# Optimization experiments

Measured on AMD Instinct MI355X. Metric: run time of the kernel, lower is better.

The kernel has to match this reference:

```python
import jax, jax.numpy as jnp
import numpy as np

B, S, D, H, DFF = 2, 2048, 1024, 16, 4096
DK = D // H
EPS = 1e-6


def setup_inputs() -> dict:
    key = jax.random.key(0)
    ks = jax.random.split(key, 16)
    s = lambda fan_in: 1.0 / np.sqrt(fan_in)
    inp = {
        "xb": jax.random.normal(ks[0], (B, S, D), jnp.float32),
        "mask": jnp.ones((B, 1, 1, S), jnp.int32),
        "Wq": jax.random.normal(ks[1], (D, D), jnp.float32) * s(D),
        "bq": jnp.zeros((D,), jnp.float32),
        "Wk": jax.random.normal(ks[2], (D, D), jnp.float32) * s(D),
        "bk": jnp.zeros((D,), jnp.float32),
        "Wv": jax.random.normal(ks[3], (D, D), jnp.float32) * s(D),
        "bv": jnp.zeros((D,), jnp.float32),
        "Wo": jax.random.normal(ks[4], (D, D), jnp.float32) * s(D),
        "bo": jnp.zeros((D,), jnp.float32),
        "W1": jax.random.normal(ks[5], (D, DFF), jnp.float32) * s(D),
        "b1": jnp.zeros((DFF,), jnp.float32),
        "W2": jax.random.normal(ks[6], (DFF, D), jnp.float32) * s(DFF),
        "b2": jnp.zeros((D,), jnp.float32),
        "a1": jnp.ones((1,), jnp.float32),
        "o1": jnp.zeros((1,), jnp.float32),
        "a2": jnp.ones((1,), jnp.float32),
        "o2": jnp.zeros((1,), jnp.float32),
    }
    return inp


def layernorm(x, alpha, bias):
    # matches LayerNormalization: unbiased std (torch default), scalar alpha/bias,
    # division by (std + eps)
    mean = jnp.mean(x, axis=-1, keepdims=True)
    var = jnp.sum((x - mean) ** 2, axis=-1, keepdims=True) / (x.shape[-1] - 1)
    std = jnp.sqrt(var)
    return alpha * (x - mean) / (std + EPS) + bias


def mha(x, mask, Wq, bq, Wk, bk, Wv, bv, Wo, bo):
    b, s, d = x.shape
    q = (x @ Wq + bq).reshape(b, s, H, DK).transpose(0, 2, 1, 3)  # [B,H,S,DK]
    k = (x @ Wk + bk).reshape(b, s, H, DK).transpose(0, 2, 1, 3)
    v = (x @ Wv + bv).reshape(b, s, H, DK).transpose(0, 2, 1, 3)
    logits = jnp.einsum("bhqd,bhkd->bhqk", q, k) / np.sqrt(DK)
    logits = jnp.where(mask == 0, jnp.float32(-1e9), logits)
    probs = jax.nn.softmax(logits, axis=-1)
    a = jnp.einsum("bhqk,bhkd->bhqd", probs, v)  # [B,H,S,DK]
    a = a.transpose(0, 2, 1, 3).reshape(b, s, d)
    return a @ Wo + bo


def reference(xb, mask, Wq, bq, Wk, bk, Wv, bv, Wo, bo, W1, b1, W2, b2, a1, o1, a2, o2):
    # residual 1: x + MHA(LN(x))  (dropout disabled: eval mode)
    h = xb + mha(layernorm(xb, a1, o1), mask, Wq, bq, Wk, bk, Wv, bv, Wo, bo)
    # residual 2: h + FFN(LN(h))
    z = layernorm(h, a2, o2)
    ff = jax.nn.relu(z @ W1 + b1) @ W2 + b2
    return h + ff
```

## Files before the change

### kernel.cpp

```cpp
#include <hip/hip_runtime.h>
#include <hip/hip_bf16.h>
#include <math.h>

typedef __bf16 bf16x8 __attribute__((ext_vector_type(8)));
typedef float f32x4 __attribute__((ext_vector_type(4)));
typedef float f32x16 __attribute__((ext_vector_type(16)));
typedef unsigned short u16;

#define DEV __device__ __forceinline__

static constexpr int Bc = 2, Sc = 2048, Dc = 1024, Hc = 16, DFFc = 4096, DKc = 64;
static constexpr int Mc = Bc * Sc;
static constexpr float QSCALE = 0.125f * 1.4426950408889634f;

DEV u16 f32_to_bf16(float x) {
    unsigned u = __builtin_bit_cast(unsigned, x);
    u += 0x7FFFu + ((u >> 16) & 1u);
    return (u16)(u >> 16);
}

DEV float bf16_to_f32(u16 h) {
    return __builtin_bit_cast(float, (unsigned)h << 16);
}

DEV float exp2_fast(float x) {
    float r;
    asm("v_exp_f32 %0, %1" : "=v"(r) : "v"(x));
    return r;
}

DEV unsigned cvt_pk_bf16(float lo, float hi_) {
    unsigned r;
    asm("v_cvt_pk_bf16_f32 %0, %1, %2" : "=v"(r) : "v"(lo), "v"(hi_));
    return r;
}

DEV void gload_lds16(const u16* g, u16* l) {
    __builtin_amdgcn_global_load_lds(
        (const __attribute__((address_space(1))) void*)g,
        (__attribute__((address_space(3))) void*)l, 16, 0, 0);
}

DEV float block_reduce_sum(float v) {
    __shared__ float part[4];
    int lane = threadIdx.x & 63, w = threadIdx.x >> 6;
    #pragma unroll
    for (int m = 1; m < 64; m <<= 1) v += __shfl_xor(v, m);
    __syncthreads();
    if (lane == 0) part[w] = v;
    __syncthreads();
    return part[0] + part[1] + part[2] + part[3];
}

__global__ __launch_bounds__(256)
void ln_kernel(const float* __restrict__ x, u16* __restrict__ y,
               const float* __restrict__ alpha, const float* __restrict__ beta) {
    long row = blockIdx.x;
    const float4 v = reinterpret_cast<const float4*>(x + row * Dc)[threadIdx.x];
    float s = v.x + v.y + v.z + v.w;
    s = block_reduce_sum(s);
    float mean = s * (1.0f / Dc);
    float d0 = v.x - mean, d1 = v.y - mean, d2 = v.z - mean, d3 = v.w - mean;
    float ss = d0*d0 + d1*d1 + d2*d2 + d3*d3;
    ss = block_reduce_sum(ss);
    float stdv = sqrtf(ss / (float)(Dc - 1));
    float sc = alpha[0] / (stdv + 1e-6f);
    float bi = beta[0];
    ushort4 o;
    o.x = f32_to_bf16(d0 * sc + bi);
    o.y = f32_to_bf16(d1 * sc + bi);
    o.z = f32_to_bf16(d2 * sc + bi);
    o.w = f32_to_bf16(d3 * sc + bi);
    reinterpret_cast<ushort4*>(y + row * Dc)[threadIdx.x] = o;
}

__global__ void transpose_conv_kernel(const float* __restrict__ in, u16* __restrict__ out,
                                      int K, int N) {
    __shared__ float tile[32][33];
    int k0 = blockIdx.y * 32, n0 = blockIdx.x * 32;
    int tx = threadIdx.x, ty = threadIdx.y;
    #pragma unroll
    for (int i = 0; i < 4; i++)
        tile[ty + i*8][tx] = in[(long)(k0 + ty + i*8) * N + n0 + tx];
    __syncthreads();
    #pragma unroll
    for (int i = 0; i < 4; i++)
        out[(long)(n0 + ty + i*8) * K + k0 + tx] = f32_to_bf16(tile[tx][ty + i*8]);
}

__global__ __launch_bounds__(256)
void mbias_kernel(const int* __restrict__ mask, float* __restrict__ mbias) {
    int i = blockIdx.x * 256 + threadIdx.x;
    mbias[i] = mask[i] ? 0.f : -1e9f;
}

enum { EPI_QKV = 0, EPI_RELU = 1, EPI_RES = 2 };

template<int EPI, int BM, int BN, bool DB>
__global__ __launch_bounds__(256, 3)
void gemm_kernel(const u16* __restrict__ A, const u16* __restrict__ BT,
                 const float* __restrict__ b0, const float* __restrict__ b1,
                 const float* __restrict__ b2, void* __restrict__ outp,
                 const float* __restrict__ res, int M, int N, int K) {
    constexpr int BK = 64, RI = BM / 32, RJ = BN / 32;
    constexpr int NB = DB ? 2 : 1;
    __shared__ u16 As[NB][BM * BK];
    __shared__ u16 Bs[NB][BN * BK];
    const int tid = threadIdx.x;
    const int wave = tid >> 6, lane = tid & 63;
    const int wr = wave >> 1, wc = wave & 1;
    const int lr = lane & 15, lg = lane >> 4;
    const int m0 = blockIdx.y * BM, n0 = blockIdx.x * BN;
    const int z = blockIdx.z;
    const u16* Bz = BT + (size_t)z * N * K;
    const int srow = lane >> 3, scol = (lane & 7) * 8;

    f32x4 acc[RI][RJ] = {};

    const u16* ap[RI];
    const u16* bp[RJ];
    #pragma unroll
    for (int i = 0; i < RI; i++) ap[i] = A  + (size_t)(m0 + (wave*RI + i)*8 + srow) * K + scol;
    #pragma unroll
    for (int j = 0; j < RJ; j++) bp[j] = Bz + (size_t)(n0 + (wave*RJ + j)*8 + srow) * K + scol;

    auto stage = [&](int bi, int kt) {
        #pragma unroll
        for (int i = 0; i < RI; i++) gload_lds16(ap[i] + kt, &As[bi][(wave*RI + i) * 512]);
        #pragma unroll
        for (int j = 0; j < RJ; j++) gload_lds16(bp[j] + kt, &Bs[bi][(wave*RJ + j) * 512]);
    };
    auto compute = [&](int bi) {
        #pragma unroll
        for (int ks = 0; ks < BK; ks += 32) {
            bf16x8 a[RI], b[RJ];
            #pragma unroll
            for (int i = 0; i < RI; i++)
                a[i] = *reinterpret_cast<const bf16x8*>(&As[bi][(wr*(BM/2) + i*16 + lr) * BK + ks + lg*8]);
            #pragma unroll
            for (int j = 0; j < RJ; j++)
                b[j] = *reinterpret_cast<const bf16x8*>(&Bs[bi][(wc*(BN/2) + j*16 + lr) * BK + ks + lg*8]);
            #pragma unroll
            for (int i = 0; i < RI; i++)
                #pragma unroll
                for (int j = 0; j < RJ; j++)
                    acc[i][j] = __builtin_amdgcn_mfma_f32_16x16x32_bf16(a[i], b[j], acc[i][j], 0, 0, 0);
        }
    };

    if constexpr (DB) {
        const int nT = K / BK;
        stage(0, 0);
        __syncthreads();
        for (int t = 0; t < nT; t++) {
            const int cur = t & 1;
            if (t + 1 < nT) stage(cur ^ 1, (t + 1) * BK);
            compute(cur);
            __syncthreads();
        }
    } else {
        for (int kt = 0; kt < K; kt += BK) {
            stage(0, kt);
            __syncthreads();
            compute(0);
            __syncthreads();
        }
    }

    const float* bias = (EPI == EPI_QKV) ? (z == 0 ? b0 : z == 1 ? b1 : b2) : b0;
    #pragma unroll
    for (int i = 0; i < RI; i++) {
        #pragma unroll
        for (int j = 0; j < RJ; j++) {
            const int col = n0 + wc*(BN/2) + j*16 + lr;
            const float bv = bias[col];
            #pragma unroll
            for (int rg = 0; rg < 4; rg++) {
                const int row = m0 + wr*(BM/2) + i*16 + lg*4 + rg;
                float val = acc[i][j][rg] + bv;
                if constexpr (EPI == EPI_QKV) {
                    int bb = row >> 11, s = row & (Sc - 1);
                    int hh = col >> 6, dk = col & 63;
                    u16* o = (u16*)outp + (size_t)z * Mc * Dc;
                    if (z == 2)
                        o[((size_t)(bb * Hc + hh) * DKc + dk) * Sc + s] = f32_to_bf16(val);
                    else
                        o[(((size_t)(bb * Hc + hh) * Sc + s) << 6) + dk] =
                            f32_to_bf16(z == 0 ? val * QSCALE : val);
                } else if constexpr (EPI == EPI_RELU) {
                    ((u16*)outp)[(size_t)row * N + col] = f32_to_bf16(fmaxf(val, 0.0f));
                } else {
                    size_t idx = (size_t)row * N + col;
                    ((float*)outp)[idx] = res[idx] + val;
                }
            }
        }
    }
}

__global__ __launch_bounds__(256, 4)
void attn_kernel(const u16* __restrict__ Qg, const u16* __restrict__ Kg,
                 const u16* __restrict__ VTg, const float* __restrict__ mbias,
                 u16* __restrict__ part, float2* __restrict__ ml) {
    constexpr int KVB = 64, NT = (Sc / 2) / KVB;
    __shared__ u16 Ks[2][KVB * DKc];
    __shared__ u16 VTs[2][KVB * DKc];
    __shared__ float mbs[Sc / 2];

    const int tid = threadIdx.x;
    const int wave = tid >> 6, lane = tid & 63;
    const int l31 = lane & 31, hi = lane >> 5;
    const int bh = blockIdx.y, b = bh >> 4, hh = bh & 15;
    const int q0 = blockIdx.x * 128 + wave * 32;
    const int z = blockIdx.z, kv0 = z * (Sc / 2);
    const long base = (long)bh * Sc * DKc;

    *reinterpret_cast<float4*>(&mbs[tid * 4]) =
        *reinterpret_cast<const float4*>(&mbias[b * Sc + kv0 + tid * 4]);

    bf16x8 qf[4];
    {
        const u16* qrow = Qg + base + (long)(q0 + l31) * DKc + hi * 8;
        #pragma unroll
        for (int s = 0; s < 4; s++)
            qf[s] = *reinterpret_cast<const bf16x8*>(qrow + s * 16);
    }

    const int unit0 = wave * 128 + lane;
    const int r0 = unit0 >> 3, u0 = unit0 & 7;
    const int c8 = (u0 ^ (r0 & 7)) * 8;
    const u16* ksrc = Kg  + base + (size_t)(kv0 + r0) * DKc + c8;
    const u16* vsrc = VTg + base + (size_t)r0 * Sc + kv0 + c8;

    auto stage = [&](int bi, int kt) {
        gload_lds16(ksrc + (size_t)kt * DKc,       &Ks [bi][wave * 1024]);
        gload_lds16(ksrc + (size_t)(kt + 8) * DKc, &Ks [bi][wave * 1024 + 512]);
        gload_lds16(vsrc + kt,                     &VTs[bi][wave * 1024]);
        gload_lds16(vsrc + kt + 8 * Sc,            &VTs[bi][wave * 1024 + 512]);
    };

    stage(0, 0);
    __syncthreads();

    f32x16 accO[2] = {};
    float mrun = -3.0e38f, lrun = 0.f;

    for (int t = 0; t < NT; t++) {
        const int cur = t & 1;
        if (t + 1 < NT) stage(cur ^ 1, (t + 1) * KVB);

        f32x16 st[2];
        #pragma unroll
        for (int kt2 = 0; kt2 < 2; kt2++) {
            f32x16 s = {};
            const int row = kt2 * 32 + l31;
            #pragma unroll
            for (int step = 0; step < 4; step++) {
                const int unit = (step * 2 + hi) ^ (row & 7);
                bf16x8 kf = *reinterpret_cast<const bf16x8*>(&Ks[cur][row * DKc + unit * 8]);
                s = __builtin_amdgcn_mfma_f32_32x32x16_bf16(kf, qf[step], s, 0, 0, 0);
            }
            st[kt2] = s;
        }

        float pm = -3.0e38f;
        #pragma unroll
        for (int kt2 = 0; kt2 < 2; kt2++) {
            #pragma unroll
            for (int g = 0; g < 4; g++) {
                const float4 mb = *reinterpret_cast<const float4*>(
                    &mbs[t * KVB + kt2 * 32 + g * 8 + hi * 4]);
                st[kt2][g*4+0] += mb.x;
                st[kt2][g*4+1] += mb.y;
                st[kt2][g*4+2] += mb.z;
                st[kt2][g*4+3] += mb.w;
                pm = fmaxf(fmaxf(pm, st[kt2][g*4+0]), st[kt2][g*4+1]);
                pm = fmaxf(fmaxf(pm, st[kt2][g*4+2]), st[kt2][g*4+3]);
            }
        }
        pm = fmaxf(pm, __shfl_xor(pm, 32));

        if (__any(pm - mrun > 11.54f)) {
            const float mnew = fmaxf(mrun, pm);
            const float corr = exp2_fast(mrun - mnew);
            mrun = mnew; lrun *= corr;
            #pragma unroll
            for (int r = 0; r < 16; r++) {
                accO[0][r] *= corr;
                accO[1][r] *= corr;
            }
        }

        float rsum = 0.f;
        #pragma unroll
        for (int kt2 = 0; kt2 < 2; kt2++)
            #pragma unroll
            for (int r = 0; r < 16; r++) {
                const float p = exp2_fast(st[kt2][r] - mrun);
                st[kt2][r] = p;
                rsum += p;
            }
        rsum += __shfl_xor(rsum, 32);
        lrun += rsum;

        #pragma unroll
        for (int kt2 = 0; kt2 < 2; kt2++) {
            #pragma unroll
            for (int kstep = 0; kstep < 2; kstep++) {
                unsigned w0 = cvt_pk_bf16(st[kt2][kstep*8+0], st[kt2][kstep*8+1]);
                unsigned w1 = cvt_pk_bf16(st[kt2][kstep*8+2], st[kt2][kstep*8+3]);
                unsigned w2 = cvt_pk_bf16(st[kt2][kstep*8+4], st[kt2][kstep*8+5]);
                unsigned w3 = cvt_pk_bf16(st[kt2][kstep*8+6], st[kt2][kstep*8+7]);
                const unsigned p0 = (unsigned)__shfl_xor((int)w0, 32);
                const unsigned p1 = (unsigned)__shfl_xor((int)w1, 32);
                const unsigned p2 = (unsigned)__shfl_xor((int)w2, 32);
                const unsigned p3 = (unsigned)__shfl_xor((int)w3, 32);
                uint4 e;
                e.x = hi ? p2 : w0;
                e.y = hi ? p3 : w1;
                e.z = hi ? w2 : p0;
                e.w = hi ? w3 : p1;
                const bf16x8 pa = __builtin_bit_cast(bf16x8, e);
                #pragma unroll
                for (int dt = 0; dt < 2; dt++) {
                    const int drow = dt * 32 + l31;
                    const int unit = (kt2 * 4 + kstep * 2 + hi) ^ (drow & 7);
                    bf16x8 vf = *reinterpret_cast<const bf16x8*>(&VTs[cur][drow * DKc + unit * 8]);
                    accO[dt] = __builtin_amdgcn_mfma_f32_32x32x16_bf16(pa, vf, accO[dt], 0, 0, 0);
                }
            }
        }
        __syncthreads();
    }

    u16* pz = part + (size_t)z * Mc * Dc;
    #pragma unroll
    for (int r = 0; r < 16; r++) {
        const int qr = (r & 3) + 8 * (r >> 2) + 4 * hi;
        u16* po = pz + ((long)(b * Sc + q0 + qr)) * Dc + hh * 64;
        po[l31]      = f32_to_bf16(accO[0][r]);
        po[32 + l31] = f32_to_bf16(accO[1][r]);
    }
    if (hi == 0)
        ml[((size_t)z * Bc * Hc + bh) * Sc + q0 + l31] = float2{mrun, lrun};
}

__global__ __launch_bounds__(256)
void combine_kernel(const u16* __restrict__ part, const float2* __restrict__ ml,
                    u16* __restrict__ Aout) {
    const int idx = blockIdx.x * 256 + threadIdx.x;
    const int row = idx >> 7, g = idx & 127, d0 = g * 8;
    const int b = row >> 11, s = row & (Sc - 1), hh = d0 >> 6;
    const int bh = b * Hc + hh;
    const float2 ab0 = ml[(size_t)bh * Sc + s];
    const float2 ab1 = ml[((size_t)Bc * Hc + bh) * Sc + s];
    const float m = fmaxf(ab0.x, ab1.x);
    const float w0 = exp2_fast(ab0.x - m), w1 = exp2_fast(ab1.x - m);
    const float rinv = 1.0f / (w0 * ab0.y + w1 * ab1.y);
    const uint4 pa = *reinterpret_cast<const uint4*>(part + (size_t)row * Dc + d0);
    const uint4 pb = *reinterpret_cast<const uint4*>(part + (size_t)Mc * Dc + (size_t)row * Dc + d0);
    const u16* ha = (const u16*)&pa;
    const u16* hb = (const u16*)&pb;
    ushort4 o[2];
    #pragma unroll
    for (int h = 0; h < 2; h++) {
        #pragma unroll
        for (int e = 0; e < 4; e++) {
            float v = (w0 * bf16_to_f32(ha[h*4+e]) + w1 * bf16_to_f32(hb[h*4+e])) * rinv;
            (&o[h].x)[e] = f32_to_bf16(v);
        }
    }
    *reinterpret_cast<ushort4*>(Aout + (size_t)row * Dc + d0)     = o[0];
    *reinterpret_cast<ushort4*>(Aout + (size_t)row * Dc + d0 + 4) = o[1];
}

extern "C" void kernel_launch(void* const* d_in, const int* in_sizes, int n_in,
                              void* d_out, int out_size, void* d_ws, size_t ws_size,
                              hipStream_t stream) {
    (void)in_sizes; (void)n_in; (void)out_size; (void)ws_size;
    const float* xb = (const float*)d_in[0];
    const int*  mask = (const int*)d_in[1];
    const float* Wq = (const float*)d_in[2];
    const float* bq = (const float*)d_in[3];
    const float* Wk = (const float*)d_in[4];
    const float* bk = (const float*)d_in[5];
    const float* Wv = (const float*)d_in[6];
    const float* bv = (const float*)d_in[7];
    const float* Wo = (const float*)d_in[8];
    const float* bo = (const float*)d_in[9];
    const float* W1 = (const float*)d_in[10];
    const float* b1 = (const float*)d_in[11];
    const float* W2 = (const float*)d_in[12];
    const float* b2 = (const float*)d_in[13];
    const float* a1 = (const float*)d_in[14];
    const float* o1 = (const float*)d_in[15];
    const float* a2 = (const float*)d_in[16];
    const float* o2 = (const float*)d_in[17];
    float* out = (float*)d_out;

    char* p = (char*)d_ws;
    auto alloc = [&](size_t bytes) { char* r = p; p += (bytes + 255) & ~(size_t)255; return r; };
    u16* xln   = (u16*)alloc((size_t)Mc * Dc * 2);
    u16* WTqkv = (u16*)alloc((size_t)3 * Dc * Dc * 2);
    u16* WTo   = (u16*)alloc((size_t)Dc * Dc * 2);
    u16* WT1   = (u16*)alloc((size_t)Dc * DFFc * 2);
    u16* WT2   = (u16*)alloc((size_t)DFFc * Dc * 2);
    u16* qkv   = (u16*)alloc((size_t)3 * Mc * Dc * 2);
    u16* Aat   = (u16*)alloc((size_t)Mc * Dc * 2);
    float* hbuf = (float*)alloc((size_t)Mc * Dc * 4);
    u16* zb  = (u16*)alloc((size_t)Mc * Dc * 2);
    u16* ffh = (u16*)alloc((size_t)Mc * DFFc * 2);

    u16*    apart = (u16*)ffh;
    float2* aml   = (float2*)hbuf;
    float*  mbias = (float*)((char*)hbuf + (size_t)2 * 1024 * 1024);

    dim3 blkT(32, 8);
    transpose_conv_kernel<<<dim3(Dc/32,   Dc/32),   blkT, 0, stream>>>(Wq, WTqkv,             Dc, Dc);
    transpose_conv_kernel<<<dim3(Dc/32,   Dc/32),   blkT, 0, stream>>>(Wk, WTqkv + Dc*Dc,     Dc, Dc);
    transpose_conv_kernel<<<dim3(Dc/32,   Dc/32),   blkT, 0, stream>>>(Wv, WTqkv + 2*Dc*Dc,   Dc, Dc);
    transpose_conv_kernel<<<dim3(Dc/32,   Dc/32),   blkT, 0, stream>>>(Wo, WTo, Dc, Dc);
    transpose_conv_kernel<<<dim3(DFFc/32, Dc/32),   blkT, 0, stream>>>(W1, WT1, Dc, DFFc);
    transpose_conv_kernel<<<dim3(Dc/32,   DFFc/32), blkT, 0, stream>>>(W2, WT2, DFFc, Dc);

    mbias_kernel<<<(Bc * Sc) / 256, 256, 0, stream>>>(mask, mbias);
    ln_kernel<<<Mc, 256, 0, stream>>>(xb, xln, a1, o1);

    gemm_kernel<EPI_QKV, 128, 128, false><<<dim3(Dc/128, Mc/128, 3), 256, 0, stream>>>(
        xln, WTqkv, bq, bk, bv, qkv, nullptr, Mc, Dc, Dc);

    attn_kernel<<<dim3(Sc/128, Bc*Hc, 2), 256, 0, stream>>>(
        qkv, qkv + (size_t)Mc*Dc, qkv + (size_t)2*Mc*Dc, mbias, apart, aml);

    combine_kernel<<<(Mc * Dc / 8) / 256, 256, 0, stream>>>(apart, aml, Aat);

    gemm_kernel<EPI_RES, 128, 64, true><<<dim3(Dc/64, Mc/128), 256, 0, stream>>>(
        Aat, WTo, bo, nullptr, nullptr, hbuf, xb, Mc, Dc, Dc);

    ln_kernel<<<Mc, 256, 0, stream>>>(hbuf, zb, a2, o2);

    gemm_kernel<EPI_RELU, 128, 128, false><<<dim3(DFFc/128, Mc/128), 256, 0, stream>>>(
        zb, WT1, b1, nullptr, nullptr, ffh, nullptr, Mc, DFFc, Dc);

    gemm_kernel<EPI_RES, 128, 64, true><<<dim3(Dc/64, Mc/128), 256, 0, stream>>>(
        ffh, WT2, b2, nullptr, nullptr, out, hbuf, Mc, Dc, DFFc);
}
```

Before: 279.9 us.

## Split the FF2 GEMM along K into two partials plus a combine kernel

The second FFN GEMM (K=4096, N=1024) now runs as two half-K GEMMs, launched via blockIdx.z, that write bf16 partial sums into the free qkv buffer. A new elementwise kernel then adds both partials, the bias and the residual. The aim is to double the block count of a long-K, narrow-N GEMM to improve CU occupancy. In exchange it adds an extra launch and partial-buffer traffic, and rounding the partials to bf16 loses some precision.

```diff
diff --git a/kernel.cpp b/kernel.cpp
--- a/kernel.cpp
+++ b/kernel.cpp
@@ -94,9 +94,9 @@
     mbias[i] = mask[i] ? 0.f : -1e9f;
 }
 
-enum { EPI_QKV = 0, EPI_RELU = 1, EPI_RES = 2 };
-
-template<int EPI, int BM, int BN, bool DB>
+enum { EPI_QKV = 0, EPI_RELU = 1, EPI_RES = 2, EPI_PART = 3 };
+
+template<int EPI, int BM, int BN, bool DB, bool SPLITK = false>
 __global__ __launch_bounds__(256, 3)
 void gemm_kernel(const u16* __restrict__ A, const u16* __restrict__ BT,
                  const float* __restrict__ b0, const float* __restrict__ b1,
@@ -112,7 +112,9 @@
     const int lr = lane & 15, lg = lane >> 4;
     const int m0 = blockIdx.y * BM, n0 = blockIdx.x * BN;
     const int z = blockIdx.z;
-    const u16* Bz = BT + (size_t)z * N * K;
+    const u16* Bz = (EPI == EPI_QKV) ? BT + (size_t)z * N * K : BT;
+    const int Keff  = SPLITK ? K / 2 : K;
+    const int k0off = SPLITK ? z * Keff : 0;
     const int srow = lane >> 3, scol = (lane & 7) * 8;
 
     f32x4 acc[RI][RJ] = {};
@@ -149,18 +151,18 @@
     };
 
     if constexpr (DB) {
-        const int nT = K / BK;
-        stage(0, 0);
+        const int nT = Keff / BK;
+        stage(0, k0off);
         __syncthreads();
         for (int t = 0; t < nT; t++) {
             const int cur = t & 1;
-            if (t + 1 < nT) stage(cur ^ 1, (t + 1) * BK);
+            if (t + 1 < nT) stage(cur ^ 1, k0off + (t + 1) * BK);
             compute(cur);
             __syncthreads();
         }
     } else {
-        for (int kt = 0; kt < K; kt += BK) {
-            stage(0, kt);
+        for (int kt = 0; kt < Keff; kt += BK) {
+            stage(0, k0off + kt);
             __syncthreads();
             compute(0);
             __syncthreads();
@@ -173,7 +175,7 @@
         #pragma unroll
         for (int j = 0; j < RJ; j++) {
             const int col = n0 + wc*(BN/2) + j*16 + lr;
-            const float bv = bias[col];
+            const float bv = (EPI == EPI_PART) ? 0.f : bias[col];
             #pragma unroll
             for (int rg = 0; rg < 4; rg++) {
                 const int row = m0 + wr*(BM/2) + i*16 + lg*4 + rg;
@@ -189,6 +191,8 @@
                             f32_to_bf16(z == 0 ? val * QSCALE : val);
                 } else if constexpr (EPI == EPI_RELU) {
                     ((u16*)outp)[(size_t)row * N + col] = f32_to_bf16(fmaxf(val, 0.0f));
+                } else if constexpr (EPI == EPI_PART) {
+                    ((u16*)outp)[(size_t)z * M * N + (size_t)row * N + col] = f32_to_bf16(val);
                 } else {
                     size_t idx = (size_t)row * N + col;
                     ((float*)outp)[idx] = res[idx] + val;
@@ -196,6 +200,33 @@
             }
         }
     }
+}
+
+__global__ __launch_bounds__(256)
+void ff2_combine_kernel(const u16* __restrict__ p0, const u16* __restrict__ p1,
+                        const float* __restrict__ bias, const float* __restrict__ res,
+                        float* __restrict__ out) {
+    const size_t e0 = ((size_t)blockIdx.x * 256 + threadIdx.x) * 8;
+    const int col = (int)(e0 & (Dc - 1));
+    const uint4 a = *reinterpret_cast<const uint4*>(p0 + e0);
+    const uint4 b = *reinterpret_cast<const uint4*>(p1 + e0);
+    const u16* ha = (const u16*)&a;
+    const u16* hb = (const u16*)&b;
+    const float4 r0 = *reinterpret_cast<const float4*>(res + e0);
+    const float4 r1 = *reinterpret_cast<const float4*>(res + e0 + 4);
+    const float4 bi0 = *reinterpret_cast<const float4*>(bias + col);
+    const float4 bi1 = *reinterpret_cast<const float4*>(bias + col + 4);
+    float4 o0, o1;
+    o0.x = r0.x + bf16_to_f32(ha[0]) + bf16_to_f32(hb[0]) + bi0.x;
+    o0.y = r0.y + bf16_to_f32(ha[1]) + bf16_to_f32(hb[1]) + bi0.y;
+    o0.z = r0.z + bf16_to_f32(ha[2]) + bf16_to_f32(hb[2]) + bi0.z;
+    o0.w = r0.w + bf16_to_f32(ha[3]) + bf16_to_f32(hb[3]) + bi0.w;
+    o1.x = r1.x + bf16_to_f32(ha[4]) + bf16_to_f32(hb[4]) + bi1.x;
+    o1.y = r1.y + bf16_to_f32(ha[5]) + bf16_to_f32(hb[5]) + bi1.y;
+    o1.z = r1.z + bf16_to_f32(ha[6]) + bf16_to_f32(hb[6]) + bi1.z;
+    o1.w = r1.w + bf16_to_f32(ha[7]) + bf16_to_f32(hb[7]) + bi1.w;
+    *reinterpret_cast<float4*>(out + e0)     = o0;
+    *reinterpret_cast<float4*>(out + e0 + 4) = o1;
 }
 
 __global__ __launch_bounds__(256, 4)
@@ -414,6 +445,7 @@
     u16*    apart = (u16*)ffh;
     float2* aml   = (float2*)hbuf;
     float*  mbias = (float*)((char*)hbuf + (size_t)2 * 1024 * 1024);
+    u16*    ff2p  = (u16*)qkv;
 
     dim3 blkT(32, 8);
     transpose_conv_kernel<<<dim3(Dc/32,   Dc/32),   blkT, 0, stream>>>(Wq, WTqkv,             Dc, Dc);
@@ -442,6 +474,9 @@
     gemm_kernel<EPI_RELU, 128, 128, false><<<dim3(DFFc/128, Mc/128), 256, 0, stream>>>(
         zb, WT1, b1, nullptr, nullptr, ffh, nullptr, Mc, DFFc, Dc);
 
-    gemm_kernel<EPI_RES, 128, 64, true><<<dim3(Dc/64, Mc/128), 256, 0, stream>>>(
-        ffh, WT2, b2, nullptr, nullptr, out, hbuf, Mc, Dc, DFFc);
-}
+    gemm_kernel<EPI_PART, 128, 64, true, true><<<dim3(Dc/64, Mc/128, 2), 256, 0, stream>>>(
+        ffh, WT2, nullptr, nullptr, nullptr, ff2p, nullptr, Mc, Dc, DFFc);
+
+    ff2_combine_kernel<<<(Mc * Dc / 8) / 256, 256, 0, stream>>>(
+        ff2p, ff2p + (size_t)Mc * Dc, b2, hbuf, out);
+}
```

Measured after the change: 295.1 us. +5.4%, slower.
